# Kernel tuning notes

Measured on AMD Instinct MI355X. Metric: run time of the kernel, lower is better.

The kernel has to match this reference:

```python
import jax, jax.numpy as jnp
import numpy as np

N = 10000      # nodes
E = 640000     # edges
P = 500000     # OD training pairs
IN, HID, EMB = 128, 256, 64


def _graph_conv(x, W, b, src, dst, norm_out, norm_in):
    # DGL GraphConv, norm='both': y = D_in^{-1/2} A (D_out^{-1/2} x) W + b
    h = x * norm_out[:, None]
    agg = jax.ops.segment_sum(h[src], dst, num_segments=N)  # [N, d]
    return agg * norm_in[:, None] @ W + b


def setup_inputs() -> dict:
    key = jax.random.key(0)
    ks = jax.random.split(key, 13)
    x = jax.random.normal(ks[0], (N, IN), jnp.float32)
    dis = jax.random.uniform(ks[1], (N, N), jnp.float32)
    src = jax.random.randint(ks[2], (E,), 0, N, dtype=jnp.int64)
    dst = jax.random.randint(ks[3], (E,), 0, N, dtype=jnp.int64)
    train_idx = jax.random.randint(ks[4], (2, P), 0, N, dtype=jnp.int64)

    def w(k, i, o):
        return (jax.random.normal(k, (i, o), jnp.float32) / np.sqrt(i)).astype(jnp.float32)

    return {
        'x': x, 'dis': dis,
        'W1': w(ks[5], IN, HID),  'b1': jnp.zeros((HID,), jnp.float32),
        'W2': w(ks[6], HID, HID), 'b2': jnp.zeros((HID,), jnp.float32),
        'W3': w(ks[7], HID, EMB), 'b3': jnp.zeros((EMB,), jnp.float32),
        'Wout': w(ks[8], 2 * EMB + 1, 1), 'bout': jnp.zeros((1,), jnp.float32),
        'src': src, 'dst': dst, 'train_idx': train_idx,
    }


def reference(x, dis, W1, b1, W2, b2, W3, b3, Wout, bout, src, dst, train_idx):
    ones = jnp.ones((E,), x.dtype)
    deg_out = jax.ops.segment_sum(ones, src, num_segments=N)
    deg_in = jax.ops.segment_sum(ones, dst, num_segments=N)
    norm_out = jnp.where(deg_out > 0, jax.lax.rsqrt(jnp.maximum(deg_out, 1.0)), 0.0)
    norm_in = jnp.where(deg_in > 0, jax.lax.rsqrt(jnp.maximum(deg_in, 1.0)), 0.0)

    h = jax.nn.relu(_graph_conv(x, W1, b1, src, dst, norm_out, norm_in))
    h = jax.nn.relu(_graph_conv(h, W2, b2, src, dst, norm_out, norm_in))
    g_emb = jax.nn.sigmoid(_graph_conv(h, W3, b3, src, dst, norm_out, norm_in))  # [N, EMB]

    o_emb = g_emb[train_idx[0]]                      # [P, EMB]
    d_emb = g_emb[train_idx[1]]                      # [P, EMB]
    dis_emb = dis[train_idx[0], train_idx[1]][:, None]  # [P, 1]
    emb = jnp.concatenate((o_emb, d_emb, dis_emb), axis=1)  # [P, 2*EMB+1]
    return jnp.tanh(emb @ Wout + bout)               # [P, 1]
```

## Files before the change

kernel.cpp:

```cpp
#include <hip/hip_runtime.h>
#include <math.h>

typedef __attribute__((ext_vector_type(8))) short short8;
typedef __attribute__((ext_vector_type(8))) unsigned short ushort8;
typedef __attribute__((ext_vector_type(4))) float f32x4;

#define NTHR 256
#define CAP 192

__device__ __forceinline__ ushort f2bf(float f) {
    uint u = __float_as_uint(f);
    return (ushort)((u + 0x7FFFu + ((u >> 16) & 1u)) >> 16);
}
__device__ __forceinline__ uint pk2bf(float a, float b) {
    return (uint)f2bf(a) | ((uint)f2bf(b) << 16);
}
__device__ __forceinline__ float bfl(uint r) { return __uint_as_float(r << 16); }
__device__ __forceinline__ float bfh(uint r) { return __uint_as_float(r & 0xFFFF0000u); }

struct Params {
    const float* x; const float* dis;
    const float* W1; const float* b1;
    const float* W2; const float* b2;
    const float* W3; const float* b3;
    const float* Wout; const float* bout;
    const int* src; const int* dst; const int* ti;
    float* out;
    uint* degOut; uint* fill;
    float* normOut; float* normIn;
    ushort* ebkt;
    ushort* xbf; ushort* w1bf; ushort* w2bf; ushort* w3bf;
    ushort* bufA; ushort* bufB; ushort* bufC;
    float* av; float* bv;
    int N, E, P;
};

__global__ __launch_bounds__(NTHR) void k_pre(Params p) {
    int gtid = blockIdx.x * NTHR + threadIdx.x;
    int GSZ = gridDim.x * NTHR;
    for (int i = gtid; i < p.N; i += GSZ) {
        p.degOut[i] = 0u;
        p.fill[i] = 0u;
    }
    uint pat = (uint)p.N | ((uint)p.N << 16);
    uint* eb = (uint*)p.ebkt;
    int nE2 = p.N * (CAP / 2);
    for (int i = gtid; i < nE2; i += GSZ) eb[i] = pat;
    if (gtid < 64) ((uint*)&p.xbf[(size_t)p.N * 128])[gtid & 31] = 0u;
    if (gtid >= 64 && gtid < 128) ((uint*)&p.bufC[(size_t)p.N * 64])[gtid & 15] = 0u;
    if (gtid >= 128 && gtid < 192) ((uint*)&p.bufB[(size_t)p.N * 256])[gtid & 63] = 0u;
}

__global__ __launch_bounds__(NTHR) void k_deg_scatter(Params p) {
    int e = blockIdx.x * NTHR + threadIdx.x;
    if (e < p.E) {
        int s = p.src[e];
        int v = p.dst[e];
        atomicAdd(&p.degOut[s], 1u);
        uint pos = atomicAdd(&p.fill[v], 1u);
        p.ebkt[(size_t)v * CAP + pos] = (ushort)s;
    }
}

__global__ __launch_bounds__(NTHR) void k_norm_cvt(Params p) {
    int gtid = blockIdx.x * NTHR + threadIdx.x;
    int GSZ = gridDim.x * NTHR;
    for (int v = gtid; v < p.N; v += GSZ) {
        uint d0 = p.degOut[v];
        uint d1 = p.fill[v];
        p.normOut[v] = d0 ? rsqrtf((float)d0) : 0.f;
        p.normIn[v] = d1 ? rsqrtf((float)d1) : 0.f;
    }
    int nx4 = p.N * 32;
    for (int i4 = gtid; i4 < nx4; i4 += GSZ) {
        int i = i4 * 4;
        int row = i >> 7;
        uint d0 = p.degOut[row];
        float no = d0 ? rsqrtf((float)d0) : 0.f;
        float4 v = *(const float4*)&p.x[i];
        uint2 pkv;
        pkv.x = pk2bf(v.x * no, v.y * no);
        pkv.y = pk2bf(v.z * no, v.w * no);
        *(uint2*)&p.xbf[i] = pkv;
    }
    const int n1 = 128 * 256, n2 = 256 * 256, n3 = 256 * 64;
    int nw4 = (n1 + n2 + n3) >> 2;
    for (int i4 = gtid; i4 < nw4; i4 += GSZ) {
        int i = i4 * 4;
        const float* s;
        ushort* d;
        int off;
        if (i < n1) { s = p.W1; d = p.w1bf; off = i; }
        else if (i < n1 + n2) { s = p.W2; d = p.w2bf; off = i - n1; }
        else { s = p.W3; d = p.w3bf; off = i - n1 - n2; }
        float4 v = *(const float4*)&s[off];
        uint2 pkv;
        pkv.x = pk2bf(v.x, v.y);
        pkv.y = pk2bf(v.z, v.w);
        *(uint2*)&d[off] = pkv;
    }
}

template <int V> struct GT;
template <> struct GT<1> { using T = ushort; };
template <> struct GT<2> { using T = uint; };

template <int V>
__device__ __forceinline__ void accum(float* acc, typename GT<V>::T g) {
    if constexpr (V == 1) {
        acc[0] += bfl((uint)g);
    } else {
        acc[0] += bfl(g);
        acc[1] += bfh(g);
    }
}

template <int D, int SPLIT, int ACT>
__global__ __launch_bounds__(NTHR) void k_agg(Params p, const ushort* __restrict__ h,
                                              ushort* __restrict__ outb) {
    constexpr int V = D / (64 * SPLIT);
    using T = typename GT<V>::T;
    int wib = threadIdx.x >> 6;
    int b = blockIdx.x;
    int v, half;
    if constexpr (SPLIT == 2) {
        half = b & 1;
        v = (b >> 1) * 4 + wib;
    } else {
        half = 0;
        v = b * 4 + wib;
    }
    if (v >= p.N) return;
    int l = threadIdx.x & 63;
    const ushort* hb = h + half * (64 * V) + l * V;
    const ushort* eb = p.ebkt + (size_t)v * CAP;

    int cnt = (int)p.fill[v];
    float acc[V] = {};

    if (cnt > 0) {
        int ngrp = (cnt + 7) >> 3;
        ushort8 w = *(const ushort8*)eb;
        int g = 0;
        for (;;) {
            T gg[8];
#pragma unroll
            for (int j = 0; j < 8; ++j) gg[j] = *(const T*)&hb[(int)w[j] * D];
            ++g;
            bool more = g < ngrp;
            ushort8 wn;
            if (more) wn = *(const ushort8*)(eb + g * 8);
#pragma unroll
            for (int j = 0; j < 8; ++j) accum<V>(acc, gg[j]);
            if (!more) break;
            w = wn;
        }
    }

    float nin = p.normIn[v];
    if constexpr (ACT == 0) {
        static_assert(V == 2, "ACT0 expects V==2");
        *(uint*)&outb[(size_t)v * D + half * (64 * V) + l * V] =
            pk2bf(acc[0] * nin, acc[1] * nin);
    } else {
        float g = acc[0] * nin + p.b3[l];
        g = 1.f / (1.f + __expf(-g));
        float pa = g * p.Wout[l];
        float pb = g * p.Wout[64 + l];
#pragma unroll
        for (int off = 32; off > 0; off >>= 1) {
            pa += __shfl_down(pa, off);
            pb += __shfl_down(pb, off);
        }
        if (l == 0) {
            p.av[v] = pa;
            p.bv[v] = pb;
        }
    }
}

template <int BM, int K, bool RELU, bool BIAS, bool SCALE>
__global__ __launch_bounds__(256) void gemm_nf(const ushort* __restrict__ A,
                                               const ushort* __restrict__ B,
                                               const float* __restrict__ bias,
                                               const float* __restrict__ rowScale,
                                               ushort* __restrict__ C,
                                               int M, int Nn) {
    constexpr int WR = BM / 64;
    constexpr int LB = K + 8;
    __shared__ ushort Bs[64 * LB];

    int tid = threadIdx.x;
    int wave = tid >> 6;
    int lane = tid & 63;
    int l15 = lane & 15;
    int l4 = lane >> 4;
    int m0 = blockIdx.x * BM;
    int n0 = blockIdx.y * 64;

    {
        int j8 = (tid & 7) * 8;
#pragma unroll
        for (int kk = tid >> 3; kk < K; kk += 32) {
            short8 v = *(const short8*)&B[(size_t)kk * Nn + n0 + j8];
#pragma unroll
            for (int j = 0; j < 8; ++j) Bs[(j8 + j) * LB + kk] = (ushort)v[j];
        }
    }
    __syncthreads();

    f32x4 acc[WR][4] = {};
    int rowl[WR];
    const ushort* Ab[WR];
#pragma unroll
    for (int r = 0; r < WR; ++r) {
        rowl[r] = m0 + wave * (16 * WR) + r * 16 + l15;
        Ab[r] = A + (size_t)rowl[r] * K + l4 * 8;
    }

#pragma unroll
    for (int k0 = 0; k0 < K; k0 += 32) {
        short8 bf[4];
#pragma unroll
        for (int n = 0; n < 4; ++n)
            bf[n] = *(const short8*)&Bs[(n * 16 + l15) * LB + k0 + l4 * 8];
#pragma unroll
        for (int r = 0; r < WR; ++r) {
            short8 af = {};
            if (rowl[r] < M) af = *(const short8*)&Ab[r][k0];
#pragma unroll
            for (int n = 0; n < 4; ++n)
                acc[r][n] = __builtin_amdgcn_mfma_f32_16x16x32_bf16(af, bf[n], acc[r][n], 0, 0, 0);
        }
    }

#pragma unroll
    for (int r = 0; r < WR; ++r) {
        int rowb = m0 + wave * (16 * WR) + r * 16 + l4 * 4;
#pragma unroll
        for (int q = 0; q < 4; ++q) {
            int row = rowb + q;
            if (row >= M) continue;
            float sc = SCALE ? rowScale[row] : 1.f;
#pragma unroll
            for (int n = 0; n < 4; ++n) {
                int col = n0 + n * 16 + l15;
                float vv = acc[r][n][q];
                if (BIAS) vv += bias[col];
                if (RELU) vv = fmaxf(vv, 0.f);
                vv *= sc;
                C[(size_t)row * Nn + col] = f2bf(vv);
            }
        }
    }
}

__global__ __launch_bounds__(NTHR) void k_final(Params p) {
    int i = blockIdx.x * NTHR + threadIdx.x;
    if (i >= p.P) return;
    int o = p.ti[i];
    int d = p.ti[p.P + i];
    float s = p.av[o] + p.bv[d] + p.dis[(size_t)o * p.N + d] * p.Wout[128] + p.bout[0];
    p.out[i] = tanhf(s);
}

extern "C" void kernel_launch(void* const* d_in, const int* in_sizes, int n_in,
                              void* d_out, int out_size, void* d_ws, size_t ws_size,
                              hipStream_t stream) {
    Params prm;
    prm.x    = (const float*)d_in[0];
    prm.dis  = (const float*)d_in[1];
    prm.W1   = (const float*)d_in[2];
    prm.b1   = (const float*)d_in[3];
    prm.W2   = (const float*)d_in[4];
    prm.b2   = (const float*)d_in[5];
    prm.W3   = (const float*)d_in[6];
    prm.b3   = (const float*)d_in[7];
    prm.Wout = (const float*)d_in[8];
    prm.bout = (const float*)d_in[9];
    prm.src  = (const int*)d_in[10];
    prm.dst  = (const int*)d_in[11];
    prm.ti   = (const int*)d_in[12];
    prm.out  = (float*)d_out;

    const int IN = 128, HID = 256, EMB = 64;
    prm.N = in_sizes[0] / IN;
    prm.E = in_sizes[10];
    prm.P = in_sizes[12] / 2;
    const int N = prm.N, E = prm.E, P = prm.P;

    char* ws = (char*)d_ws;
    size_t off = 0;
    auto alloc = [&](size_t bytes) {
        size_t o = off;
        off = (off + bytes + 255) & ~(size_t)255;
        return o;
    };
    size_t o_degO = alloc((size_t)N * 4);
    size_t o_fill = alloc((size_t)N * 4);
    size_t o_nrmO = alloc((size_t)N * 4);
    size_t o_nrmI = alloc((size_t)N * 4);
    size_t o_ebkt = alloc((size_t)N * CAP * 2);
    size_t o_xbf  = alloc((size_t)(N + 1) * IN * 2);
    size_t o_w1   = alloc((size_t)IN * HID * 2);
    size_t o_w2   = alloc((size_t)HID * HID * 2);
    size_t o_w3   = alloc((size_t)HID * EMB * 2);
    size_t o_bufA = alloc((size_t)N * HID * 2);
    size_t o_bufB = alloc((size_t)(N + 1) * HID * 2);
    size_t o_bufC = alloc((size_t)(N + 1) * EMB * 2);
    size_t o_av   = alloc((size_t)N * 4);
    size_t o_bv   = alloc((size_t)N * 4);
    (void)ws_size;

    prm.degOut  = (uint*)(ws + o_degO);
    prm.fill    = (uint*)(ws + o_fill);
    prm.normOut = (float*)(ws + o_nrmO);
    prm.normIn  = (float*)(ws + o_nrmI);
    prm.ebkt    = (ushort*)(ws + o_ebkt);
    prm.xbf     = (ushort*)(ws + o_xbf);
    prm.w1bf    = (ushort*)(ws + o_w1);
    prm.w2bf    = (ushort*)(ws + o_w2);
    prm.w3bf    = (ushort*)(ws + o_w3);
    prm.bufA    = (ushort*)(ws + o_bufA);
    prm.bufB    = (ushort*)(ws + o_bufB);
    prm.bufC    = (ushort*)(ws + o_bufC);
    prm.av      = (float*)(ws + o_av);
    prm.bv      = (float*)(ws + o_bv);

    k_pre<<<1024, NTHR, 0, stream>>>(prm);
    k_deg_scatter<<<(E + NTHR - 1) / NTHR, NTHR, 0, stream>>>(prm);
    k_norm_cvt<<<1024, NTHR, 0, stream>>>(prm);

    int nb4 = (N + 3) / 4;

    k_agg<128, 1, 0><<<nb4, NTHR, 0, stream>>>(prm, prm.xbf, prm.bufA);
    {
        dim3 grid((N + 127) / 128, HID / 64);
        gemm_nf<128, 128, true, true, true><<<grid, 256, 0, stream>>>(
            prm.bufA, prm.w1bf, prm.b1, prm.normOut, prm.bufB, N, HID);
    }
    k_agg<256, 2, 0><<<nb4 * 2, NTHR, 0, stream>>>(prm, prm.bufB, prm.bufA);
    {
        dim3 grid((N + 127) / 128, HID / 64);
        gemm_nf<128, 256, true, true, true><<<grid, 256, 0, stream>>>(
            prm.bufA, prm.w2bf, prm.b2, prm.normOut, prm.bufB, N, HID);
    }
    {
        dim3 grid((N + 63) / 64, EMB / 64);
        gemm_nf<64, 256, false, false, false><<<grid, 256, 0, stream>>>(
            prm.bufB, prm.w3bf, nullptr, nullptr, prm.bufC, N, EMB);
    }
    k_agg<64, 1, 2><<<nb4, NTHR, 0, stream>>>(prm, prm.bufC, nullptr);
    k_final<<<(P + NTHR - 1) / NTHR, NTHR, 0, stream>>>(prm);
}
```

Measured before the change: 166.8 us.

## Pad edge buckets only to group boundary, pipeline gathers, vectorize scatter and final

Stops filling the whole CAP-sized edge bucket array with the sentinel and instead pads each node's bucket only up to the next multiple of 8 in the norm kernel. Weight conversion moves into the pre kernel, which now runs on fewer blocks. The aggregation loop is restructured to software-pipeline the gathers of the next 8-neighbor group before accumulating the current one. The degree scatter and final kernels each process two items per thread using int2/float2 loads and stores. This removes a large memset of roughly N*CAP*2 bytes and aims for more memory-level parallelism, at the cost of extra registers in the aggregation loop.

```diff
diff --git a/kernel.cpp b/kernel.cpp
--- a/kernel.cpp
+++ b/kernel.cpp
@@ -42,47 +42,9 @@
         p.degOut[i] = 0u;
         p.fill[i] = 0u;
     }
-    uint pat = (uint)p.N | ((uint)p.N << 16);
-    uint* eb = (uint*)p.ebkt;
-    int nE2 = p.N * (CAP / 2);
-    for (int i = gtid; i < nE2; i += GSZ) eb[i] = pat;
-    if (gtid < 64) ((uint*)&p.xbf[(size_t)p.N * 128])[gtid & 31] = 0u;
-    if (gtid >= 64 && gtid < 128) ((uint*)&p.bufC[(size_t)p.N * 64])[gtid & 15] = 0u;
-    if (gtid >= 128 && gtid < 192) ((uint*)&p.bufB[(size_t)p.N * 256])[gtid & 63] = 0u;
-}
-
-__global__ __launch_bounds__(NTHR) void k_deg_scatter(Params p) {
-    int e = blockIdx.x * NTHR + threadIdx.x;
-    if (e < p.E) {
-        int s = p.src[e];
-        int v = p.dst[e];
-        atomicAdd(&p.degOut[s], 1u);
-        uint pos = atomicAdd(&p.fill[v], 1u);
-        p.ebkt[(size_t)v * CAP + pos] = (ushort)s;
-    }
-}
-
-__global__ __launch_bounds__(NTHR) void k_norm_cvt(Params p) {
-    int gtid = blockIdx.x * NTHR + threadIdx.x;
-    int GSZ = gridDim.x * NTHR;
-    for (int v = gtid; v < p.N; v += GSZ) {
-        uint d0 = p.degOut[v];
-        uint d1 = p.fill[v];
-        p.normOut[v] = d0 ? rsqrtf((float)d0) : 0.f;
-        p.normIn[v] = d1 ? rsqrtf((float)d1) : 0.f;
-    }
-    int nx4 = p.N * 32;
-    for (int i4 = gtid; i4 < nx4; i4 += GSZ) {
-        int i = i4 * 4;
-        int row = i >> 7;
-        uint d0 = p.degOut[row];
-        float no = d0 ? rsqrtf((float)d0) : 0.f;
-        float4 v = *(const float4*)&p.x[i];
-        uint2 pkv;
-        pkv.x = pk2bf(v.x * no, v.y * no);
-        pkv.y = pk2bf(v.z * no, v.w * no);
-        *(uint2*)&p.xbf[i] = pkv;
-    }
+    if (gtid < 64) ((uint*)&p.xbf[(size_t)p.N * 128])[gtid] = 0u;
+    else if (gtid < 192) ((uint*)&p.bufB[(size_t)p.N * 256])[gtid - 64] = 0u;
+    else if (gtid < 224) ((uint*)&p.bufC[(size_t)p.N * 64])[gtid - 192] = 0u;
     const int n1 = 128 * 256, n2 = 256 * 256, n3 = 256 * 64;
     int nw4 = (n1 + n2 + n3) >> 2;
     for (int i4 = gtid; i4 < nw4; i4 += GSZ) {
@@ -101,6 +63,52 @@
     }
 }
 
+__global__ __launch_bounds__(NTHR) void k_deg_scatter(Params p) {
+    int e = (blockIdx.x * NTHR + threadIdx.x) * 2;
+    if (e + 1 < p.E) {
+        int2 s2 = *(const int2*)&p.src[e];
+        int2 d2 = *(const int2*)&p.dst[e];
+        atomicAdd(&p.degOut[s2.x], 1u);
+        atomicAdd(&p.degOut[s2.y], 1u);
+        uint p0 = atomicAdd(&p.fill[d2.x], 1u);
+        p.ebkt[(size_t)d2.x * CAP + p0] = (ushort)s2.x;
+        uint p1 = atomicAdd(&p.fill[d2.y], 1u);
+        p.ebkt[(size_t)d2.y * CAP + p1] = (ushort)s2.y;
+    } else if (e < p.E) {
+        int s = p.src[e];
+        int v = p.dst[e];
+        atomicAdd(&p.degOut[s], 1u);
+        uint pos = atomicAdd(&p.fill[v], 1u);
+        p.ebkt[(size_t)v * CAP + pos] = (ushort)s;
+    }
+}
+
+__global__ __launch_bounds__(NTHR) void k_norm_cvt(Params p) {
+    int gtid = blockIdx.x * NTHR + threadIdx.x;
+    int GSZ = gridDim.x * NTHR;
+    for (int v = gtid; v < p.N; v += GSZ) {
+        uint d0 = p.degOut[v];
+        uint d1 = p.fill[v];
+        p.normOut[v] = d0 ? rsqrtf((float)d0) : 0.f;
+        p.normIn[v] = d1 ? rsqrtf((float)d1) : 0.f;
+        uint c8 = (d1 + 7) & ~7u;
+        ushort* eb = p.ebkt + (size_t)v * CAP;
+        for (uint j = d1; j < c8; ++j) eb[j] = (ushort)p.N;
+    }
+    int nx4 = p.N * 32;
+    for (int i4 = gtid; i4 < nx4; i4 += GSZ) {
+        int i = i4 * 4;
+        int row = i >> 7;
+        uint d0 = p.degOut[row];
+        float no = d0 ? rsqrtf((float)d0) : 0.f;
+        float4 v = *(const float4*)&p.x[i];
+        uint2 pkv;
+        pkv.x = pk2bf(v.x * no, v.y * no);
+        pkv.y = pk2bf(v.z * no, v.w * no);
+        *(uint2*)&p.xbf[i] = pkv;
+    }
+}
+
 template <int V> struct GT;
 template <> struct GT<1> { using T = ushort; };
 template <> struct GT<2> { using T = uint; };
@@ -136,28 +144,29 @@
     const ushort* eb = p.ebkt + (size_t)v * CAP;
 
     int cnt = (int)p.fill[v];
+    float nin = p.normIn[v];
     float acc[V] = {};
 
     if (cnt > 0) {
         int ngrp = (cnt + 7) >> 3;
         ushort8 w = *(const ushort8*)eb;
-        int g = 0;
-        for (;;) {
-            T gg[8];
-#pragma unroll
-            for (int j = 0; j < 8; ++j) gg[j] = *(const T*)&hb[(int)w[j] * D];
-            ++g;
-            bool more = g < ngrp;
-            ushort8 wn;
-            if (more) wn = *(const ushort8*)(eb + g * 8);
-#pragma unroll
-            for (int j = 0; j < 8; ++j) accum<V>(acc, gg[j]);
-            if (!more) break;
-            w = wn;
-        }
-    }
-
-    float nin = p.normIn[v];
+        T gp[8];
+#pragma unroll
+        for (int j = 0; j < 8; ++j) gp[j] = *(const T*)&hb[(int)w[j] * D];
+        for (int g = 1; g < ngrp; ++g) {
+            ushort8 wn = *(const ushort8*)(eb + g * 8);
+            T gn[8];
+#pragma unroll
+            for (int j = 0; j < 8; ++j) gn[j] = *(const T*)&hb[(int)wn[j] * D];
+#pragma unroll
+            for (int j = 0; j < 8; ++j) accum<V>(acc, gp[j]);
+#pragma unroll
+            for (int j = 0; j < 8; ++j) gp[j] = gn[j];
+        }
+#pragma unroll
+        for (int j = 0; j < 8; ++j) accum<V>(acc, gp[j]);
+    }
+
     if constexpr (ACT == 0) {
         static_assert(V == 2, "ACT0 expects V==2");
         *(uint*)&outb[(size_t)v * D + half * (64 * V) + l * V] =
@@ -256,12 +265,24 @@
 }
 
 __global__ __launch_bounds__(NTHR) void k_final(Params p) {
-    int i = blockIdx.x * NTHR + threadIdx.x;
-    if (i >= p.P) return;
-    int o = p.ti[i];
-    int d = p.ti[p.P + i];
-    float s = p.av[o] + p.bv[d] + p.dis[(size_t)o * p.N + d] * p.Wout[128] + p.bout[0];
-    p.out[i] = tanhf(s);
+    int i = (blockIdx.x * NTHR + threadIdx.x) * 2;
+    float w128 = p.Wout[128];
+    float b0 = p.bout[0];
+    if (i + 1 < p.P) {
+        int2 o2 = *(const int2*)&p.ti[i];
+        int2 d2 = *(const int2*)&p.ti[p.P + i];
+        float dis0 = p.dis[(size_t)o2.x * p.N + d2.x];
+        float dis1 = p.dis[(size_t)o2.y * p.N + d2.y];
+        float s0 = p.av[o2.x] + p.bv[d2.x] + dis0 * w128 + b0;
+        float s1 = p.av[o2.y] + p.bv[d2.y] + dis1 * w128 + b0;
+        float2 r = make_float2(tanhf(s0), tanhf(s1));
+        *(float2*)&p.out[i] = r;
+    } else if (i < p.P) {
+        int o = p.ti[i];
+        int d = p.ti[p.P + i];
+        float s = p.av[o] + p.bv[d] + p.dis[(size_t)o * p.N + d] * w128 + b0;
+        p.out[i] = tanhf(s);
+    }
 }
 
 extern "C" void kernel_launch(void* const* d_in, const int* in_sizes, int n_in,
@@ -327,8 +348,8 @@
     prm.av      = (float*)(ws + o_av);
     prm.bv      = (float*)(ws + o_bv);
 
-    k_pre<<<1024, NTHR, 0, stream>>>(prm);
-    k_deg_scatter<<<(E + NTHR - 1) / NTHR, NTHR, 0, stream>>>(prm);
+    k_pre<<<256, NTHR, 0, stream>>>(prm);
+    k_deg_scatter<<<(E / 2 + NTHR - 1) / NTHR, NTHR, 0, stream>>>(prm);
     k_norm_cvt<<<1024, NTHR, 0, stream>>>(prm);
 
     int nb4 = (N + 3) / 4;
@@ -351,5 +372,5 @@
             prm.bufB, prm.w3bf, nullptr, nullptr, prm.bufC, N, EMB);
     }
     k_agg<64, 1, 2><<<nb4, NTHR, 0, stream>>>(prm, prm.bufC, nullptr);
-    k_final<<<(P + NTHR - 1) / NTHR, NTHR, 0, stream>>>(prm);
-}
+    k_final<<<(P / 2 + NTHR - 1) / NTHR, NTHR, 0, stream>>>(prm);
+}
```

Measured after the change: 170.0 us. Within noise of the previous version (+1.9%).
